# Kernel tuning notes

Measured on AMD Instinct MI355X. Metric: run time of the kernel, lower is better.

Reference implementation:

```python
import jax, jax.numpy as jnp
import numpy as np

GAMMA = 1.0
EPS = 1e-6
MAXITERS = 1000

B, H, W = 64, 512, 512


def setup_inputs() -> dict:
    key = jax.random.key(0)
    kM, kr, kc = jax.random.split(key, 3)
    M = jax.random.normal(kM, (B, H, W), dtype=jnp.float32)
    # r, c must be positive; uniform in [0.5, 1.5)
    r = jax.random.uniform(kr, (B, H), dtype=jnp.float32) + 0.5
    c = jax.random.uniform(kc, (B, W), dtype=jnp.float32) + 0.5
    return {"M": M, "r": r, "c": c}


def _sinkhorn(M, r, c, gamma, eps, maxiters):
    # M: (B,H,W); r: (B,H) (normalized); c: (B,W) (normalized)
    P0 = jnp.exp(-gamma * (M - jnp.min(M, axis=2, keepdims=True)))

    def cond(state):
        _, i, done = state
        return jnp.logical_and(i < maxiters, jnp.logical_not(done))

    def body(state):
        P, i, _ = state
        alpha = jnp.sum(P, axis=2)                      # (B,H) row sums
        alpha = jnp.where(alpha == 0, eps, alpha)
        P = P / alpha[:, :, None] * r[:, :, None]       # enforce row marginals
        beta = jnp.sum(P, axis=1)                       # (B,W) col sums
        beta = jnp.where(beta == 0, eps, beta)
        done = jnp.max(jnp.abs(beta - c)) <= eps        # global convergence check (as in torch)
        # torch breaks BEFORE the column update when converged
        P = jnp.where(done, P, P / beta[:, None, :] * c[:, None, :])
        return P, i + 1, done

    P, _, _ = jax.lax.while_loop(cond, body, (P0, jnp.int32(0), jnp.bool_(False)))
    return P


def reference(M, r, c):
    r_n = r / jnp.sum(r, axis=1, keepdims=True)
    c_n = c / jnp.sum(c, axis=1, keepdims=True)
    return _sinkhorn(M, r_n, c_n, GAMMA, EPS, MAXITERS)
```

## Files before the change

kernel.cpp:

```cpp
#include <hip/hip_runtime.h>
#include <hip/hip_cooperative_groups.h>

namespace cg = cooperative_groups;

namespace {
constexpr int kB = 64, kH = 512, kW = 512;
constexpr float kEps = 1e-6f;
constexpr int kMaxIt = 1000;
constexpr int kBlk = 256;
constexpr int kThr = 1024;
constexpr int kWaves = kThr / 64;
}

__device__ float    g_KTp[2][kB][4][kW];
__device__ float    g_errp[2][kB * 4];
__device__ unsigned g_leaf[8 * 16];
__device__ unsigned g_root[16];

__device__ __forceinline__ float waveRedSum(float v) {
  #pragma unroll
  for (int o = 32; o; o >>= 1) v += __shfl_xor(v, o);
  return v;
}
__device__ __forceinline__ float waveRedMax(float v) {
  #pragma unroll
  for (int o = 32; o; o >>= 1) v = fmaxf(v, __shfl_xor(v, o));
  return v;
}
__device__ __forceinline__ float waveRedMin(float v) {
  #pragma unroll
  for (int o = 32; o; o >>= 1) v = fminf(v, __shfl_xor(v, o));
  return v;
}

__device__ __forceinline__ void gbar(int t) {
  __syncthreads();
  if (threadIdx.x == 0) {
    unsigned gi = (blockIdx.x & 7) * 16;
    unsigned old = atomicAdd(&g_leaf[gi], 1u);
    if (old + 1u == 32u * (unsigned)t)
      atomicAdd(&g_root[0], 1u);
    while (__hip_atomic_load(&g_root[0], __ATOMIC_RELAXED,
                             __HIP_MEMORY_SCOPE_AGENT) < 8u * (unsigned)t) {
      __builtin_amdgcn_s_sleep(4);
    }
    asm volatile("" ::: "memory");
  }
  __syncthreads();
}

__global__ __launch_bounds__(kThr, 4)
void sinkhorn_kernel(const float* __restrict__ M, const float* __restrict__ r,
                     const float* __restrict__ c, float* __restrict__ P) {
  __shared__ float s_part[kWaves][kW];
  __shared__ float s_v[4][kW];
  __shared__ float s_cn[kW];
  __shared__ float s_rn[128];
  __shared__ float s_red[kWaves];
  __shared__ float s_bc[2];

  const int tid = threadIdx.x, bid = blockIdx.x;
  const int b = bid >> 2;
  const int q = bid & 3;
  const int w = tid >> 6, lane = tid & 63;
  const int row0 = q * 128 + w * 8;

  if (bid == 0 && tid == 0) {
    #pragma unroll
    for (int i = 0; i < 8; ++i) atomicExch(&g_leaf[i * 16], 0u);
    atomicExch(&g_root[0], 0u);
  }
  if (tid == 0)
    __hip_atomic_store(&g_errp[0][bid], __builtin_inff(),
                       __ATOMIC_RELAXED, __HIP_MEMORY_SCOPE_AGENT);
  cg::this_grid().sync();

  {
    float rv = (tid < kH) ? r[(size_t)b * kH + tid] : 0.f;
    float ws = waveRedSum(rv);
    if (lane == 0) s_red[w] = ws;
    __syncthreads();
    if (tid == 0) {
      float s = s_red[0];
      #pragma unroll
      for (int i = 1; i < kWaves; ++i) s += s_red[i];
      s_bc[0] = s;
    }
    __syncthreads();
    float rsum = s_bc[0];
    if (tid < 128) s_rn[tid] = r[(size_t)b * kH + q * 128 + tid] / rsum;
    __syncthreads();

    float cv = (tid < kW) ? c[(size_t)b * kW + tid] : 0.f;
    ws = waveRedSum(cv);
    if (lane == 0) s_red[w] = ws;
    __syncthreads();
    if (tid == 0) {
      float s = s_red[0];
      #pragma unroll
      for (int i = 1; i < kWaves; ++i) s += s_red[i];
      s_bc[0] = s;
    }
    __syncthreads();
    float csum = s_bc[0];
    if (tid < kW) {
      s_cn[tid] = c[(size_t)b * kW + tid] / csum;
      s_v[1][tid] = 1.0f;
    }
  }

  float4 kreg[8][2];
  #pragma unroll
  for (int rr = 0; rr < 8; ++rr) {
    const float4* Mr = (const float4*)(M + ((size_t)b * kH + row0 + rr) * kW);
    float4 a = Mr[lane], d = Mr[64 + lane];
    float mn = fminf(fminf(fminf(a.x, a.y), fminf(a.z, a.w)),
                     fminf(fminf(d.x, d.y), fminf(d.z, d.w)));
    mn = waveRedMin(mn);
    float4 ka, kb;
    ka.x = expf(mn - a.x); ka.y = expf(mn - a.y);
    ka.z = expf(mn - a.z); ka.w = expf(mn - a.w);
    kb.x = expf(mn - d.x); kb.y = expf(mn - d.y);
    kb.z = expf(mn - d.z); kb.w = expf(mn - d.w);
    kreg[rr][0] = ka; kreg[rr][1] = kb;
  }
  __syncthreads();

  float u_prev[8], u_cur[8];
  #pragma unroll
  for (int i = 0; i < 8; ++i) u_prev[i] = 1.f;

  int fin_vslot = 0;
  int t = 1;
  for (;; ++t) {
    const int p = t & 3;
    const int h = t & 1;
    const float4* v4 = (const float4*)s_v[p];
    float4 va = v4[lane], vb = v4[64 + lane];
    float4 cp0 = make_float4(0.f, 0.f, 0.f, 0.f);
    float4 cp1 = make_float4(0.f, 0.f, 0.f, 0.f);
    #pragma unroll
    for (int rr = 0; rr < 8; ++rr) {
      float4 k0 = kreg[rr][0], k1 = kreg[rr][1];
      float s = k0.x * va.x + k0.y * va.y + k0.z * va.z + k0.w * va.w +
                k1.x * vb.x + k1.y * vb.y + k1.z * vb.z + k1.w * vb.w;
      s = waveRedSum(s);
      float up = u_prev[rr];
      float al = up * s;
      al = (al == 0.f) ? kEps : al;
      float un = up / al * s_rn[w * 8 + rr];
      u_cur[rr] = un;
      cp0.x = fmaf(un, k0.x, cp0.x); cp0.y = fmaf(un, k0.y, cp0.y);
      cp0.z = fmaf(un, k0.z, cp0.z); cp0.w = fmaf(un, k0.w, cp0.w);
      cp1.x = fmaf(un, k1.x, cp1.x); cp1.y = fmaf(un, k1.y, cp1.y);
      cp1.z = fmaf(un, k1.z, cp1.z); cp1.w = fmaf(un, k1.w, cp1.w);
    }
    float4* pp = (float4*)&s_part[w][0];
    pp[lane] = cp0; pp[64 + lane] = cp1;
    __syncthreads();
    if (tid < kW) {
      float s = 0.f;
      #pragma unroll
      for (int ww = 0; ww < kWaves; ++ww) s += s_part[ww][tid];
      __hip_atomic_store(&g_KTp[h][b][q][tid], s,
                         __ATOMIC_RELAXED, __HIP_MEMORY_SCOPE_AGENT);
    }

    gbar(t);

    float err = 0.f;
    if (tid < kW) {
      float kt = 0.f;
      #pragma unroll
      for (int qq = 0; qq < 4; ++qq)
        kt += __hip_atomic_load(&g_KTp[h][b][qq][tid],
                                __ATOMIC_RELAXED, __HIP_MEMORY_SCOPE_AGENT);
      float vt = s_v[p][tid];
      float beta = vt * kt;
      beta = (beta == 0.f) ? kEps : beta;
      float cn = s_cn[tid];
      s_v[(t + 1) & 3][tid] = vt / beta * cn;
      err = fabsf(beta - cn);
    }
    err = waveRedMax(err);
    if (lane == 0) s_red[w] = err;
    __syncthreads();
    if (tid == 0) {
      float mx = s_red[0];
      #pragma unroll
      for (int i = 1; i < kWaves; ++i) mx = fmaxf(mx, s_red[i]);
      __hip_atomic_store(&g_errp[h][bid], mx,
                         __ATOMIC_RELAXED, __HIP_MEMORY_SCOPE_AGENT);
    }
    __syncthreads();

    float gv = 0.f;
    if (tid < kBlk) {
      gv = __hip_atomic_load(&g_errp[(t - 1) & 1][tid],
                             __ATOMIC_RELAXED, __HIP_MEMORY_SCOPE_AGENT);
    }
    gv = waveRedMax(gv);
    if (lane == 0 && w < 4) s_red[w] = gv;
    __syncthreads();
    gv = fmaxf(fmaxf(s_red[0], s_red[1]), fmaxf(s_red[2], s_red[3]));

    if (gv <= kEps) {
      fin_vslot = (t - 1) & 3;
      break;
    }
    if (t == kMaxIt + 1) {
      fin_vslot = t & 3;
      break;
    }
    #pragma unroll
    for (int i = 0; i < 8; ++i) u_prev[i] = u_cur[i];
  }

  const float4* vf4 = (const float4*)s_v[fin_vslot];
  float4 vfa = vf4[lane], vfb = vf4[64 + lane];
  #pragma unroll
  for (int rr = 0; rr < 8; ++rr) {
    float4 k0 = kreg[rr][0], k1 = kreg[rr][1];
    float un = u_prev[rr];
    k0.x = un * k0.x * vfa.x; k0.y = un * k0.y * vfa.y;
    k0.z = un * k0.z * vfa.z; k0.w = un * k0.w * vfa.w;
    k1.x = un * k1.x * vfb.x; k1.y = un * k1.y * vfb.y;
    k1.z = un * k1.z * vfb.z; k1.w = un * k1.w * vfb.w;
    float4* Pr = (float4*)(P + ((size_t)b * kH + row0 + rr) * kW);
    Pr[lane] = k0; Pr[64 + lane] = k1;
  }
}

extern "C" void kernel_launch(void* const* d_in, const int* in_sizes, int n_in,
                              void* d_out, int out_size, void* d_ws, size_t ws_size,
                              hipStream_t stream) {
  (void)in_sizes; (void)n_in; (void)d_ws; (void)ws_size; (void)out_size;
  const float* M = (const float*)d_in[0];
  const float* r = (const float*)d_in[1];
  const float* c = (const float*)d_in[2];
  float* P = (float*)d_out;
  void* args[] = { (void*)&M, (void*)&r, (void*)&c, (void*)&P };
  hipLaunchCooperativeKernel((const void*)sinkhorn_kernel, dim3(kBlk), dim3(kThr),
                             args, 0, stream);
}
```

Measured before the change: 255.8 us.

## Replace grid-wide barrier with per-batch flag sync and lagged global convergence check

Swaps the grid-wide tree barrier for a per-batch handshake: the four blocks of one batch publish and poll iteration tags, so each batch advances without waiting on all 256 blocks. The global convergence test now reads per-batch error values tagged with an iteration two steps back, and u/v history is kept in small shared ring buffers so the final scaling can roll back to the converged slot. This removes the all-block barrier latency from every iteration. In exchange it adds tag polling, one extra lagged iteration, and memory-ordering subtleties with relaxed atomics and a manual waitcnt.

```diff
diff --git a/kernel.cpp b/kernel.cpp
--- a/kernel.cpp
+++ b/kernel.cpp
@@ -9,13 +9,13 @@
 constexpr int kMaxIt = 1000;
 constexpr int kBlk = 256;
 constexpr int kThr = 1024;
-constexpr int kWaves = kThr / 64;
+constexpr int kWaves = 16;
 }
 
 __device__ float    g_KTp[2][kB][4][kW];
-__device__ float    g_errp[2][kB * 4];
-__device__ unsigned g_leaf[8 * 16];
-__device__ unsigned g_root[16];
+__device__ float    g_err[8][kB];
+__device__ unsigned g_etag[kB];
+__device__ unsigned g_ptag[kB][16];
 
 __device__ __forceinline__ float waveRedSum(float v) {
   #pragma unroll
@@ -31,22 +31,6 @@
   #pragma unroll
   for (int o = 32; o; o >>= 1) v = fminf(v, __shfl_xor(v, o));
   return v;
-}
-
-__device__ __forceinline__ void gbar(int t) {
-  __syncthreads();
-  if (threadIdx.x == 0) {
-    unsigned gi = (blockIdx.x & 7) * 16;
-    unsigned old = atomicAdd(&g_leaf[gi], 1u);
-    if (old + 1u == 32u * (unsigned)t)
-      atomicAdd(&g_root[0], 1u);
-    while (__hip_atomic_load(&g_root[0], __ATOMIC_RELAXED,
-                             __HIP_MEMORY_SCOPE_AGENT) < 8u * (unsigned)t) {
-      __builtin_amdgcn_s_sleep(4);
-    }
-    asm volatile("" ::: "memory");
-  }
-  __syncthreads();
 }
 
 __global__ __launch_bounds__(kThr, 4)
@@ -54,6 +38,7 @@
                      const float* __restrict__ c, float* __restrict__ P) {
   __shared__ float s_part[kWaves][kW];
   __shared__ float s_v[4][kW];
+  __shared__ float s_u[4][128];
   __shared__ float s_cn[kW];
   __shared__ float s_rn[128];
   __shared__ float s_red[kWaves];
@@ -65,14 +50,11 @@
   const int w = tid >> 6, lane = tid & 63;
   const int row0 = q * 128 + w * 8;
 
-  if (bid == 0 && tid == 0) {
-    #pragma unroll
-    for (int i = 0; i < 8; ++i) atomicExch(&g_leaf[i * 16], 0u);
-    atomicExch(&g_root[0], 0u);
-  }
-  if (tid == 0)
-    __hip_atomic_store(&g_errp[0][bid], __builtin_inff(),
-                       __ATOMIC_RELAXED, __HIP_MEMORY_SCOPE_AGENT);
+  if (tid == 0) {
+    __hip_atomic_store(&g_ptag[b][q], 0u, __ATOMIC_RELAXED, __HIP_MEMORY_SCOPE_AGENT);
+    if (q == 0)
+      __hip_atomic_store(&g_etag[b], 0u, __ATOMIC_RELAXED, __HIP_MEMORY_SCOPE_AGENT);
+  }
   cg::this_grid().sync();
 
   {
@@ -107,6 +89,7 @@
       s_cn[tid] = c[(size_t)b * kW + tid] / csum;
       s_v[1][tid] = 1.0f;
     }
+    if (tid < 128) s_u[0][tid] = 1.0f;
   }
 
   float4 kreg[8][2];
@@ -126,26 +109,22 @@
   }
   __syncthreads();
 
-  float u_prev[8], u_cur[8];
-  #pragma unroll
-  for (int i = 0; i < 8; ++i) u_prev[i] = 1.f;
-
-  int fin_vslot = 0;
-  int t = 1;
-  for (;; ++t) {
+  int fin_u_slot = 0, fin_v_slot = 0;
+  for (int t = 1;; ++t) {
     const int p = t & 3;
     const int h = t & 1;
     const float4* v4 = (const float4*)s_v[p];
     float4 va = v4[lane], vb = v4[64 + lane];
     float4 cp0 = make_float4(0.f, 0.f, 0.f, 0.f);
     float4 cp1 = make_float4(0.f, 0.f, 0.f, 0.f);
+    float u_cur[8];
     #pragma unroll
     for (int rr = 0; rr < 8; ++rr) {
       float4 k0 = kreg[rr][0], k1 = kreg[rr][1];
       float s = k0.x * va.x + k0.y * va.y + k0.z * va.z + k0.w * va.w +
                 k1.x * vb.x + k1.y * vb.y + k1.z * vb.z + k1.w * vb.w;
       s = waveRedSum(s);
-      float up = u_prev[rr];
+      float up = s_u[(t - 1) & 3][w * 8 + rr];
       float al = up * s;
       al = (al == 0.f) ? kEps : al;
       float un = up / al * s_rn[w * 8 + rr];
@@ -155,6 +134,10 @@
       cp1.x = fmaf(un, k1.x, cp1.x); cp1.y = fmaf(un, k1.y, cp1.y);
       cp1.z = fmaf(un, k1.z, cp1.z); cp1.w = fmaf(un, k1.w, cp1.w);
     }
+    if (lane == 0) {
+      #pragma unroll
+      for (int rr = 0; rr < 8; ++rr) s_u[p][w * 8 + rr] = u_cur[rr];
+    }
     float4* pp = (float4*)&s_part[w][0];
     pp[lane] = cp0; pp[64 + lane] = cp1;
     __syncthreads();
@@ -165,9 +148,33 @@
       __hip_atomic_store(&g_KTp[h][b][q][tid], s,
                          __ATOMIC_RELAXED, __HIP_MEMORY_SCOPE_AGENT);
     }
-
-    gbar(t);
-
+    __syncthreads();
+    if (tid == 0)
+      __hip_atomic_store(&g_ptag[b][q], (unsigned)t,
+                         __ATOMIC_RELAXED, __HIP_MEMORY_SCOPE_AGENT);
+    if (w == 0) {
+      for (;;) {
+        unsigned tg = (unsigned)t;
+        if (lane < 4)
+          tg = __hip_atomic_load(&g_ptag[b][lane],
+                                 __ATOMIC_RELAXED, __HIP_MEMORY_SCOPE_AGENT);
+        if (__all(tg >= (unsigned)t)) break;
+        __builtin_amdgcn_s_sleep(1);
+      }
+    } else if (w == 15 && t >= 3) {
+      unsigned need = (unsigned)(t - 2);
+      for (;;) {
+        unsigned tg = __hip_atomic_load(&g_etag[lane],
+                                        __ATOMIC_RELAXED, __HIP_MEMORY_SCOPE_AGENT);
+        if (__all(tg >= need)) break;
+        __builtin_amdgcn_s_sleep(1);
+      }
+      float e = __hip_atomic_load(&g_err[(t - 2) & 7][lane],
+                                  __ATOMIC_RELAXED, __HIP_MEMORY_SCOPE_AGENT);
+      e = waveRedMax(e);
+      if (lane == 0) s_bc[1] = e;
+    }
+    __syncthreads();
     float err = 0.f;
     if (tid < kW) {
       float kt = 0.f;
@@ -185,43 +192,37 @@
     err = waveRedMax(err);
     if (lane == 0) s_red[w] = err;
     __syncthreads();
-    if (tid == 0) {
+    if (tid == 0 && q == 0) {
       float mx = s_red[0];
       #pragma unroll
       for (int i = 1; i < kWaves; ++i) mx = fmaxf(mx, s_red[i]);
-      __hip_atomic_store(&g_errp[h][bid], mx,
-                         __ATOMIC_RELAXED, __HIP_MEMORY_SCOPE_AGENT);
-    }
-    __syncthreads();
-
-    float gv = 0.f;
-    if (tid < kBlk) {
-      gv = __hip_atomic_load(&g_errp[(t - 1) & 1][tid],
-                             __ATOMIC_RELAXED, __HIP_MEMORY_SCOPE_AGENT);
-    }
-    gv = waveRedMax(gv);
-    if (lane == 0 && w < 4) s_red[w] = gv;
-    __syncthreads();
-    gv = fmaxf(fmaxf(s_red[0], s_red[1]), fmaxf(s_red[2], s_red[3]));
-
-    if (gv <= kEps) {
-      fin_vslot = (t - 1) & 3;
+      __hip_atomic_store(&g_err[t & 7][b], mx,
+                         __ATOMIC_RELAXED, __HIP_MEMORY_SCOPE_AGENT);
+      asm volatile("s_waitcnt vmcnt(0)" ::: "memory");
+      __hip_atomic_store(&g_etag[b], (unsigned)t,
+                         __ATOMIC_RELAXED, __HIP_MEMORY_SCOPE_AGENT);
+    }
+    if (t >= 3 && s_bc[1] <= kEps) {
+      fin_u_slot = (t - 2) & 3;
+      fin_v_slot = (t - 2) & 3;
       break;
     }
-    if (t == kMaxIt + 1) {
-      fin_vslot = t & 3;
+    if (t == kMaxIt + 2) {
+      fin_u_slot = kMaxIt & 3;
+      fin_v_slot = (kMaxIt + 1) & 3;
       break;
     }
-    #pragma unroll
-    for (int i = 0; i < 8; ++i) u_prev[i] = u_cur[i];
-  }
-
-  const float4* vf4 = (const float4*)s_v[fin_vslot];
+  }
+
+  float ufin[8];
+  #pragma unroll
+  for (int rr = 0; rr < 8; ++rr) ufin[rr] = s_u[fin_u_slot][w * 8 + rr];
+  const float4* vf4 = (const float4*)s_v[fin_v_slot];
   float4 vfa = vf4[lane], vfb = vf4[64 + lane];
   #pragma unroll
   for (int rr = 0; rr < 8; ++rr) {
     float4 k0 = kreg[rr][0], k1 = kreg[rr][1];
-    float un = u_prev[rr];
+    float un = ufin[rr];
     k0.x = un * k0.x * vfa.x; k0.y = un * k0.y * vfa.y;
     k0.z = un * k0.z * vfa.z; k0.w = un * k0.w * vfa.w;
     k1.x = un * k1.x * vfb.x; k1.y = un * k1.y * vfb.y;
```

Result: no change. 258.3 us (+1.0%).
